# Optimization experiments

Hardware: AMD Instinct MI355X
Metric: run time of the kernel (lower is better)

Reference implementation:

```python
import jax, jax.numpy as jnp
import numpy as np

NUM_USERS = 200000
NUM_ITEMS = 100000
N_NODES = NUM_USERS + NUM_ITEMS
EMB_DIM = 64
N_LAYERS = 3
NNZ = 5000000


def setup_inputs() -> dict:
    key = jax.random.key(0)
    k1, k2, k3, k4, k5 = jax.random.split(key, 5)
    user_emb = 0.1 * jax.random.normal(k1, (NUM_USERS, EMB_DIM), dtype=jnp.float32)
    item_emb = 0.1 * jax.random.normal(k2, (NUM_ITEMS, EMB_DIM), dtype=jnp.float32)
    edge_row = jax.random.randint(k3, (NNZ,), 0, N_NODES, dtype=jnp.int32)
    edge_col = jax.random.randint(k4, (NNZ,), 0, N_NODES, dtype=jnp.int32)
    edge_val = jax.random.uniform(k5, (NNZ,), dtype=jnp.float32)
    return {"user_emb": user_emb, "item_emb": item_emb,
            "edge_row": edge_row, "edge_col": edge_col, "edge_val": edge_val}


def _spmm(edge_row, edge_col, edge_val, x):
    # out[r] = sum_{e: row[e]=r} val[e] * x[col[e]]  (COO SpMM)
    msgs = edge_val[:, None] * x[edge_col]  # [nnz, d]
    return jax.ops.segment_sum(msgs, edge_row, num_segments=N_NODES)


def reference(user_emb, item_emb, edge_row, edge_col, edge_val):
    ego = jnp.concatenate([user_emb, item_emb], axis=0)  # [N, d]
    acc = ego
    h = ego
    for _ in range(N_LAYERS):
        h = _spmm(edge_row, edge_col, edge_val, h)
        acc = acc + h
    mean_emb = acc / jnp.asarray(N_LAYERS + 1, dtype=acc.dtype)
    return mean_emb[:NUM_USERS], mean_emb[NUM_USERS:]
```

## Files before the change

kernel.cpp:

```cpp
#include <hip/hip_runtime.h>
#include <hip/hip_fp16.h>
#include <hip/hip_bf16.h>


#define NUM_USERS 200000
#define NUM_ITEMS 100000
#define N_NODES   300000
#define EMB_DIM   64
#define NNZ       5000000

#define COARSE_SHIFT 10
#define COARSE_ROWS  1024
#define NCOARSE      ((N_NODES + COARSE_ROWS - 1) / COARSE_ROWS)

#define ARENA_CAP 24576

#define P1_CHUNK  16384
#define P1_BLOCKS ((NNZ + P1_CHUNK - 1) / P1_CHUNK)

__global__ void init16_kernel(const float4* __restrict__ user_emb,
                              const float4* __restrict__ item_emb,
                              uint2* __restrict__ h16) {
    const int n4 = N_NODES * (EMB_DIM / 4);
    int idx = blockIdx.x * blockDim.x + threadIdx.x;
    if (idx >= n4) return;
    const int user4 = NUM_USERS * (EMB_DIM / 4);
    float4 v = (idx < user4) ? user_emb[idx] : item_emb[idx - user4];
    __half2 p0 = __floats2half2_rn(v.x, v.y);
    __half2 p1 = __floats2half2_rn(v.z, v.w);
    uint2 u;
    u.x = *(unsigned int*)&p0;
    u.y = *(unsigned int*)&p1;
    h16[idx] = u;
}

__global__ void zero_int_kernel(int* __restrict__ p, int n) {
    int idx = blockIdx.x * blockDim.x + threadIdx.x;
    if (idx < n) p[idx] = 0;
}

__global__ void partition_arena(const int* __restrict__ row,
                                const int* __restrict__ col,
                                const float* __restrict__ val,
                                int* __restrict__ ccur,
                                unsigned long long* __restrict__ arena) {
    __shared__ int hist[NCOARSE];
    __shared__ int lbase[NCOARSE];
    __shared__ int lcur[NCOARSE];
    int t = threadIdx.x;
    int start = blockIdx.x * P1_CHUNK;
    int end = min(start + P1_CHUNK, NNZ);
    for (int j = t; j < NCOARSE; j += 256) { hist[j] = 0; lcur[j] = 0; }
    __syncthreads();
    for (int i = start + t; i < end; i += 256)
        atomicAdd(&hist[(unsigned int)row[i] >> COARSE_SHIFT], 1);
    __syncthreads();
    for (int j = t; j < NCOARSE; j += 256) {
        int c = hist[j];
        if (c > 0)
            lbase[j] = j * ARENA_CAP + atomicAdd(&ccur[j], c);
    }
    __syncthreads();
    for (int i = start + t; i < end; i += 256) {
        int r = row[i];
        int b = (int)((unsigned int)r >> COARSE_SHIFT);
        unsigned int lo = ((unsigned int)col[i] << 10) | ((unsigned int)r & 1023u);
        unsigned long long p = ((unsigned long long)__float_as_uint(val[i]) << 32)
                             | (unsigned long long)lo;
        int pos = lbase[b] + atomicAdd(&lcur[b], 1);
        arena[pos] = p;
    }
}

__global__ void arena_scan(const int* __restrict__ cnt, int* __restrict__ cbase) {
    __shared__ int lds[512];
    int t = threadIdx.x;
    lds[t] = (t < NCOARSE) ? cnt[t] : 0;
    __syncthreads();
    for (int off = 1; off < 512; off <<= 1) {
        int v = (t >= off) ? lds[t - off] : 0;
        __syncthreads();
        lds[t] += v;
        __syncthreads();
    }
    if (t < NCOARSE) cbase[t] = (t > 0) ? lds[t - 1] : 0;
    if (t == 0) cbase[NCOARSE] = lds[NCOARSE - 1];
}

__global__ void __launch_bounds__(1024)
fine_scatter(const int* __restrict__ cbase,
             const int* __restrict__ cnt,
             const unsigned long long* __restrict__ arena,
             unsigned long long* __restrict__ csr,
             int* __restrict__ row_ptr) {
    __shared__ int offs[COARSE_ROWS];
    __shared__ int cur[COARSE_ROWS];
    int t = threadIdx.x;
    int bin = blockIdx.x;
    int n = cnt[bin];
    int cstart = cbase[bin];
    const unsigned long long* src = arena + (size_t)bin * ARENA_CAP;
    offs[t] = 0;
    cur[t] = 0;
    __syncthreads();
    for (int i = t; i < n; i += 1024)
        atomicAdd(&offs[(unsigned int)src[i] & 1023u], 1);
    __syncthreads();
    int c = offs[t];
    for (int off = 1; off < 1024; off <<= 1) {
        int v = (t >= off) ? offs[t - off] : 0;
        __syncthreads();
        offs[t] += v;
        __syncthreads();
    }
    int excl = offs[t] - c;
    __syncthreads();
    offs[t] = excl;
    __syncthreads();
    int r = (bin << COARSE_SHIFT) + t;
    if (r < N_NODES) row_ptr[r] = cstart + excl;
    if (bin == NCOARSE - 1 && t == 0) row_ptr[N_NODES] = cbase[NCOARSE];
    for (int i = t; i < n; i += 1024) {
        unsigned long long p = src[i];
        int rl = (int)((unsigned int)p & 1023u);
        int pos = cstart + offs[rl] + atomicAdd(&cur[rl], 1);
        csr[pos] = p;
    }
}

__global__ void spmm_mid_kernel(const int* __restrict__ row_ptr,
                                const unsigned long long* __restrict__ csr,
                                const __half* __restrict__ x,
                                __half* __restrict__ y) {
    int gid  = blockIdx.x * blockDim.x + threadIdx.x;
    int wid  = gid >> 6;
    int lane = threadIdx.x & 63;
    if (wid >= N_NODES) return;
    wid = __builtin_amdgcn_readfirstlane(wid);
    int s = row_ptr[wid];
    int e = row_ptr[wid + 1];
    float acc = 0.f;
    int k = s;
    for (; k + 8 <= e; k += 8) {
        unsigned long long p0 = csr[k];
        unsigned long long p1 = csr[k + 1];
        unsigned long long p2 = csr[k + 2];
        unsigned long long p3 = csr[k + 3];
        unsigned long long p4 = csr[k + 4];
        unsigned long long p5 = csr[k + 5];
        unsigned long long p6 = csr[k + 6];
        unsigned long long p7 = csr[k + 7];
        float x0 = __half2float(x[(((unsigned int)p0 >> 10) << 6) + lane]);
        float x1 = __half2float(x[(((unsigned int)p1 >> 10) << 6) + lane]);
        float x2 = __half2float(x[(((unsigned int)p2 >> 10) << 6) + lane]);
        float x3 = __half2float(x[(((unsigned int)p3 >> 10) << 6) + lane]);
        float x4 = __half2float(x[(((unsigned int)p4 >> 10) << 6) + lane]);
        float x5 = __half2float(x[(((unsigned int)p5 >> 10) << 6) + lane]);
        float x6 = __half2float(x[(((unsigned int)p6 >> 10) << 6) + lane]);
        float x7 = __half2float(x[(((unsigned int)p7 >> 10) << 6) + lane]);
        acc += __uint_as_float((unsigned int)(p0 >> 32)) * x0;
        acc += __uint_as_float((unsigned int)(p1 >> 32)) * x1;
        acc += __uint_as_float((unsigned int)(p2 >> 32)) * x2;
        acc += __uint_as_float((unsigned int)(p3 >> 32)) * x3;
        acc += __uint_as_float((unsigned int)(p4 >> 32)) * x4;
        acc += __uint_as_float((unsigned int)(p5 >> 32)) * x5;
        acc += __uint_as_float((unsigned int)(p6 >> 32)) * x6;
        acc += __uint_as_float((unsigned int)(p7 >> 32)) * x7;
    }
    for (; k + 4 <= e; k += 4) {
        unsigned long long p0 = csr[k];
        unsigned long long p1 = csr[k + 1];
        unsigned long long p2 = csr[k + 2];
        unsigned long long p3 = csr[k + 3];
        float x0 = __half2float(x[(((unsigned int)p0 >> 10) << 6) + lane]);
        float x1 = __half2float(x[(((unsigned int)p1 >> 10) << 6) + lane]);
        float x2 = __half2float(x[(((unsigned int)p2 >> 10) << 6) + lane]);
        float x3 = __half2float(x[(((unsigned int)p3 >> 10) << 6) + lane]);
        acc += __uint_as_float((unsigned int)(p0 >> 32)) * x0;
        acc += __uint_as_float((unsigned int)(p1 >> 32)) * x1;
        acc += __uint_as_float((unsigned int)(p2 >> 32)) * x2;
        acc += __uint_as_float((unsigned int)(p3 >> 32)) * x3;
    }
    for (; k < e; ++k) {
        unsigned long long p = csr[k];
        acc += __uint_as_float((unsigned int)(p >> 32))
             * __half2float(x[(((unsigned int)p >> 10) << 6) + lane]);
    }
    y[(wid << 6) + lane] = __float2half(acc);
}

__global__ void spmm_last_kernel(const int* __restrict__ row_ptr,
                                 const unsigned long long* __restrict__ csr,
                                 const __half* __restrict__ x,
                                 const __half* __restrict__ h1,
                                 const float* __restrict__ user_emb,
                                 const float* __restrict__ item_emb,
                                 float* __restrict__ out) {
    int gid  = blockIdx.x * blockDim.x + threadIdx.x;
    int wid  = gid >> 6;
    int lane = threadIdx.x & 63;
    if (wid >= N_NODES) return;
    wid = __builtin_amdgcn_readfirstlane(wid);
    int s = row_ptr[wid];
    int e = row_ptr[wid + 1];
    float acc = 0.f;
    int k = s;
    for (; k + 8 <= e; k += 8) {
        unsigned long long p0 = csr[k];
        unsigned long long p1 = csr[k + 1];
        unsigned long long p2 = csr[k + 2];
        unsigned long long p3 = csr[k + 3];
        unsigned long long p4 = csr[k + 4];
        unsigned long long p5 = csr[k + 5];
        unsigned long long p6 = csr[k + 6];
        unsigned long long p7 = csr[k + 7];
        float x0 = __half2float(x[(((unsigned int)p0 >> 10) << 6) + lane]);
        float x1 = __half2float(x[(((unsigned int)p1 >> 10) << 6) + lane]);
        float x2 = __half2float(x[(((unsigned int)p2 >> 10) << 6) + lane]);
        float x3 = __half2float(x[(((unsigned int)p3 >> 10) << 6) + lane]);
        float x4 = __half2float(x[(((unsigned int)p4 >> 10) << 6) + lane]);
        float x5 = __half2float(x[(((unsigned int)p5 >> 10) << 6) + lane]);
        float x6 = __half2float(x[(((unsigned int)p6 >> 10) << 6) + lane]);
        float x7 = __half2float(x[(((unsigned int)p7 >> 10) << 6) + lane]);
        acc += __uint_as_float((unsigned int)(p0 >> 32)) * x0;
        acc += __uint_as_float((unsigned int)(p1 >> 32)) * x1;
        acc += __uint_as_float((unsigned int)(p2 >> 32)) * x2;
        acc += __uint_as_float((unsigned int)(p3 >> 32)) * x3;
        acc += __uint_as_float((unsigned int)(p4 >> 32)) * x4;
        acc += __uint_as_float((unsigned int)(p5 >> 32)) * x5;
        acc += __uint_as_float((unsigned int)(p6 >> 32)) * x6;
        acc += __uint_as_float((unsigned int)(p7 >> 32)) * x7;
    }
    for (; k + 4 <= e; k += 4) {
        unsigned long long p0 = csr[k];
        unsigned long long p1 = csr[k + 1];
        unsigned long long p2 = csr[k + 2];
        unsigned long long p3 = csr[k + 3];
        float x0 = __half2float(x[(((unsigned int)p0 >> 10) << 6) + lane]);
        float x1 = __half2float(x[(((unsigned int)p1 >> 10) << 6) + lane]);
        float x2 = __half2float(x[(((unsigned int)p2 >> 10) << 6) + lane]);
        float x3 = __half2float(x[(((unsigned int)p3 >> 10) << 6) + lane]);
        acc += __uint_as_float((unsigned int)(p0 >> 32)) * x0;
        acc += __uint_as_float((unsigned int)(p1 >> 32)) * x1;
        acc += __uint_as_float((unsigned int)(p2 >> 32)) * x2;
        acc += __uint_as_float((unsigned int)(p3 >> 32)) * x3;
    }
    for (; k < e; ++k) {
        unsigned long long p = csr[k];
        acc += __uint_as_float((unsigned int)(p >> 32))
             * __half2float(x[(((unsigned int)p >> 10) << 6) + lane]);
    }
    int o = (wid << 6) + lane;
    float h0v = (o < NUM_USERS * EMB_DIM) ? user_emb[o]
                                          : item_emb[o - NUM_USERS * EMB_DIM];
    float h1v = __half2float(h1[o]);
    float h2v = __half2float(x[o]);
    __builtin_nontemporal_store((h0v + h1v + h2v + acc) * 0.25f, &out[o]);
}

__global__ void init32_kernel(const float4* __restrict__ user_emb,
                              const float4* __restrict__ item_emb,
                              float4* __restrict__ h,
                              float4* __restrict__ out) {
    const int n4 = N_NODES * (EMB_DIM / 4);
    int idx = blockIdx.x * blockDim.x + threadIdx.x;
    if (idx >= n4) return;
    const int user4 = NUM_USERS * (EMB_DIM / 4);
    float4 v = (idx < user4) ? user_emb[idx] : item_emb[idx - user4];
    h[idx] = v;
    out[idx] = v;
}
__global__ void zero4_kernel(float4* __restrict__ p) {
    const int n4 = N_NODES * (EMB_DIM / 4);
    int idx = blockIdx.x * blockDim.x + threadIdx.x;
    if (idx < n4) p[idx] = make_float4(0.f, 0.f, 0.f, 0.f);
}
__global__ void spmm_push_kernel(const int* __restrict__ row, const int* __restrict__ col,
                                 const float* __restrict__ val, const float* __restrict__ x,
                                 float* __restrict__ y) {
    unsigned int gid = blockIdx.x * blockDim.x + threadIdx.x;
    unsigned int e = gid >> 6, lane = gid & 63u;
    if (e >= NNZ) return;
    atomicAdd(&y[(unsigned int)row[e] * EMB_DIM + lane],
              val[e] * x[(unsigned int)col[e] * EMB_DIM + lane]);
}
__global__ void acc_kernel(float4* __restrict__ out, const float4* __restrict__ h, float scale) {
    const int n4 = N_NODES * (EMB_DIM / 4);
    int idx = blockIdx.x * blockDim.x + threadIdx.x;
    if (idx >= n4) return;
    float4 o = out[idx], a = h[idx];
    o.x = (o.x + a.x) * scale; o.y = (o.y + a.y) * scale;
    o.z = (o.z + a.z) * scale; o.w = (o.w + a.w) * scale;
    out[idx] = o;
}

extern "C" void kernel_launch(void* const* d_in, const int* in_sizes, int n_in,
                              void* d_out, int out_size, void* d_ws, size_t ws_size,
                              hipStream_t stream) {
    const float* user_emb = (const float*)d_in[0];
    const float* item_emb = (const float*)d_in[1];
    const int*   edge_row = (const int*)d_in[2];
    const int*   edge_col = (const int*)d_in[3];
    const float* edge_val = (const float*)d_in[4];
    float* out = (float*)d_out;

    const size_t H16_BYTES = (size_t)N_NODES * EMB_DIM * sizeof(__half);

    char* ws = (char*)d_ws;
    __half* hA     = (__half*)ws;                      ws += H16_BYTES;
    __half* hB     = (__half*)ws;                      ws += H16_BYTES;
    unsigned long long* csr = (unsigned long long*)ws; ws += (size_t)NNZ * 8;
    int*   row_ptr = (int*)ws;                         ws += (size_t)(N_NODES + 4) * 4;
    int*   counts  = (int*)ws;                         ws += (size_t)N_NODES * 4;
    int*   partials= (int*)ws;                         ws += 4096;
    const size_t REQUIRED = (size_t)(ws - (char*)d_ws);

    const int blk     = 256;
    const int n4      = N_NODES * (EMB_DIM / 4);
    const int grid_n4 = (n4 + blk - 1) / blk;

    if (ws_size >= REQUIRED) {
        unsigned long long* arena = (unsigned long long*)hA;
        zero_int_kernel<<<1, 512, 0, stream>>>(counts, NCOARSE);
        partition_arena<<<P1_BLOCKS, 256, 0, stream>>>(
            edge_row, edge_col, edge_val, counts, arena);
        arena_scan<<<1, 512, 0, stream>>>(counts, partials);
        fine_scatter<<<NCOARSE, 1024, 0, stream>>>(partials, counts, arena,
                                                   csr, row_ptr);
        init16_kernel<<<grid_n4, blk, 0, stream>>>(
            (const float4*)user_emb, (const float4*)item_emb, (uint2*)hA);
        const int grid_sp = (int)(((long long)N_NODES * 64) / blk);
        spmm_mid_kernel<<<grid_sp, blk, 0, stream>>>(row_ptr, csr, hA, hB);
        spmm_mid_kernel<<<grid_sp, blk, 0, stream>>>(row_ptr, csr, hB, hA);
        spmm_last_kernel<<<grid_sp, blk, 0, stream>>>(
            row_ptr, csr, hA , hB , user_emb, item_emb, out);
    } else {
        const float scales[3] = {1.0f, 1.0f, 0.25f};
        float* hA32 = (float*)d_ws;
        float* hB32 = hA32 + (size_t)N_NODES * EMB_DIM;
        init32_kernel<<<grid_n4, blk, 0, stream>>>(
            (const float4*)user_emb, (const float4*)item_emb, (float4*)hA32, (float4*)out);
        float* h = hA32; float* hn = hB32;
        const int grid_sp = (int)(((long long)NNZ * 64) / blk);
        for (int layer = 0; layer < 3; ++layer) {
            zero4_kernel<<<grid_n4, blk, 0, stream>>>((float4*)hn);
            spmm_push_kernel<<<grid_sp, blk, 0, stream>>>(edge_row, edge_col, edge_val, h, hn);
            acc_kernel<<<grid_n4, blk, 0, stream>>>((float4*)out, (const float4*)hn, scales[layer]);
            float* t = h; h = hn; hn = t;
        }
    }
}
```

Baseline: 721.2 us.

## Pair rows per wavefront in SpMM and stage fine scatter bins in LDS

Each SpMM wavefront now handles two adjacent rows, interleaving their gather loops to raise memory-level parallelism, and launches half as many waves. The coarse bucket size drops from 1024 to 512 rows, so the column field gets one more bit, the arena capacity is halved, and the scan covers more bins. fine_scatter caches its bin's entries in dynamic shared memory so the arena is read from global memory only once. Interleaving two rows of unequal length adds tail imbalance and register pressure, and bins larger than the cache fall back to the old double-read path.

```diff
diff --git a/kernel.cpp b/kernel.cpp
--- a/kernel.cpp
+++ b/kernel.cpp
@@ -9,14 +9,18 @@
 #define EMB_DIM   64
 #define NNZ       5000000
 
-#define COARSE_SHIFT 10
-#define COARSE_ROWS  1024
+#define COARSE_SHIFT 9
+#define COARSE_ROWS  512
 #define NCOARSE      ((N_NODES + COARSE_ROWS - 1) / COARSE_ROWS)
 
-#define ARENA_CAP 24576
+#define ARENA_CAP 12288
+#define FS_CAP    9216
+#define FS_SHMEM  (FS_CAP * 8 + 2 * COARSE_ROWS * 4)
 
 #define P1_CHUNK  16384
 #define P1_BLOCKS ((NNZ + P1_CHUNK - 1) / P1_CHUNK)
+
+typedef unsigned long long u64;
 
 __global__ void init16_kernel(const float4* __restrict__ user_emb,
                               const float4* __restrict__ item_emb,
@@ -43,7 +47,7 @@
                                 const int* __restrict__ col,
                                 const float* __restrict__ val,
                                 int* __restrict__ ccur,
-                                unsigned long long* __restrict__ arena) {
+                                u64* __restrict__ arena) {
     __shared__ int hist[NCOARSE];
     __shared__ int lbase[NCOARSE];
     __shared__ int lcur[NCOARSE];
@@ -64,20 +68,20 @@
     for (int i = start + t; i < end; i += 256) {
         int r = row[i];
         int b = (int)((unsigned int)r >> COARSE_SHIFT);
-        unsigned int lo = ((unsigned int)col[i] << 10) | ((unsigned int)r & 1023u);
-        unsigned long long p = ((unsigned long long)__float_as_uint(val[i]) << 32)
-                             | (unsigned long long)lo;
+        unsigned int lo = ((unsigned int)col[i] << 9) | ((unsigned int)r & 511u);
+        u64 p = ((u64)__float_as_uint(val[i]) << 32) | (u64)lo;
         int pos = lbase[b] + atomicAdd(&lcur[b], 1);
         arena[pos] = p;
     }
 }
 
-__global__ void arena_scan(const int* __restrict__ cnt, int* __restrict__ cbase) {
-    __shared__ int lds[512];
+__global__ void __launch_bounds__(1024)
+arena_scan(const int* __restrict__ cnt, int* __restrict__ cbase) {
+    __shared__ int lds[1024];
     int t = threadIdx.x;
     lds[t] = (t < NCOARSE) ? cnt[t] : 0;
     __syncthreads();
-    for (int off = 1; off < 512; off <<= 1) {
+    for (int off = 1; off < 1024; off <<= 1) {
         int v = (t >= off) ? lds[t - off] : 0;
         __syncthreads();
         lds[t] += v;
@@ -90,74 +94,88 @@
 __global__ void __launch_bounds__(1024)
 fine_scatter(const int* __restrict__ cbase,
              const int* __restrict__ cnt,
-             const unsigned long long* __restrict__ arena,
-             unsigned long long* __restrict__ csr,
+             const u64* __restrict__ arena,
+             u64* __restrict__ csr,
              int* __restrict__ row_ptr) {
-    __shared__ int offs[COARSE_ROWS];
-    __shared__ int cur[COARSE_ROWS];
+    extern __shared__ u64 smem[];
+    u64* buf  = smem;
+    int* offs = (int*)&smem[FS_CAP];
+    int* cur  = offs + COARSE_ROWS;
     int t = threadIdx.x;
     int bin = blockIdx.x;
     int n = cnt[bin];
     int cstart = cbase[bin];
-    const unsigned long long* src = arena + (size_t)bin * ARENA_CAP;
-    offs[t] = 0;
-    cur[t] = 0;
-    __syncthreads();
-    for (int i = t; i < n; i += 1024)
-        atomicAdd(&offs[(unsigned int)src[i] & 1023u], 1);
-    __syncthreads();
-    int c = offs[t];
-    for (int off = 1; off < 1024; off <<= 1) {
-        int v = (t >= off) ? offs[t - off] : 0;
-        __syncthreads();
-        offs[t] += v;
-        __syncthreads();
-    }
-    int excl = offs[t] - c;
-    __syncthreads();
-    offs[t] = excl;
-    __syncthreads();
-    int r = (bin << COARSE_SHIFT) + t;
-    if (r < N_NODES) row_ptr[r] = cstart + excl;
-    if (bin == NCOARSE - 1 && t == 0) row_ptr[N_NODES] = cbase[NCOARSE];
-    for (int i = t; i < n; i += 1024) {
-        unsigned long long p = src[i];
-        int rl = (int)((unsigned int)p & 1023u);
-        int pos = cstart + offs[rl] + atomicAdd(&cur[rl], 1);
-        csr[pos] = p;
-    }
-}
-
-__global__ void spmm_mid_kernel(const int* __restrict__ row_ptr,
-                                const unsigned long long* __restrict__ csr,
-                                const __half* __restrict__ x,
-                                __half* __restrict__ y) {
-    int gid  = blockIdx.x * blockDim.x + threadIdx.x;
-    int wid  = gid >> 6;
-    int lane = threadIdx.x & 63;
-    if (wid >= N_NODES) return;
-    wid = __builtin_amdgcn_readfirstlane(wid);
-    int s = row_ptr[wid];
-    int e = row_ptr[wid + 1];
-    float acc = 0.f;
-    int k = s;
+    const u64* src = arena + (size_t)bin * ARENA_CAP;
+    if (t < COARSE_ROWS) { offs[t] = 0; cur[t] = 0; }
+    __syncthreads();
+    if (n <= FS_CAP) {
+        for (int i = t; i < n; i += 1024) {
+            u64 p = src[i];
+            buf[i] = p;
+            atomicAdd(&offs[(unsigned int)p & 511u], 1);
+        }
+        __syncthreads();
+        int c = (t < COARSE_ROWS) ? offs[t] : 0;
+        for (int off = 1; off < COARSE_ROWS; off <<= 1) {
+            int v = (t >= off && t < COARSE_ROWS) ? offs[t - off] : 0;
+            __syncthreads();
+            if (t < COARSE_ROWS) offs[t] += v;
+            __syncthreads();
+        }
+        int excl = (t < COARSE_ROWS) ? offs[t] - c : 0;
+        __syncthreads();
+        if (t < COARSE_ROWS) offs[t] = excl;
+        __syncthreads();
+        int r = (bin << COARSE_SHIFT) + t;
+        if (t < COARSE_ROWS && r < N_NODES) row_ptr[r] = cstart + excl;
+        if (bin == NCOARSE - 1 && t == 0) row_ptr[N_NODES] = cbase[NCOARSE];
+        for (int i = t; i < n; i += 1024) {
+            u64 p = buf[i];
+            int rl = (int)((unsigned int)p & 511u);
+            int pos = cstart + offs[rl] + atomicAdd(&cur[rl], 1);
+            csr[pos] = p;
+        }
+    } else {
+        for (int i = t; i < n; i += 1024)
+            atomicAdd(&offs[(unsigned int)src[i] & 511u], 1);
+        __syncthreads();
+        int c = (t < COARSE_ROWS) ? offs[t] : 0;
+        for (int off = 1; off < COARSE_ROWS; off <<= 1) {
+            int v = (t >= off && t < COARSE_ROWS) ? offs[t - off] : 0;
+            __syncthreads();
+            if (t < COARSE_ROWS) offs[t] += v;
+            __syncthreads();
+        }
+        int excl = (t < COARSE_ROWS) ? offs[t] - c : 0;
+        __syncthreads();
+        if (t < COARSE_ROWS) offs[t] = excl;
+        __syncthreads();
+        int r = (bin << COARSE_SHIFT) + t;
+        if (t < COARSE_ROWS && r < N_NODES) row_ptr[r] = cstart + excl;
+        if (bin == NCOARSE - 1 && t == 0) row_ptr[N_NODES] = cbase[NCOARSE];
+        for (int i = t; i < n; i += 1024) {
+            u64 p = src[i];
+            int rl = (int)((unsigned int)p & 511u);
+            int pos = cstart + offs[rl] + atomicAdd(&cur[rl], 1);
+            csr[pos] = p;
+        }
+    }
+}
+
+__device__ __forceinline__ void tail_accum(const u64* __restrict__ csr,
+                                           const __half* __restrict__ x,
+                                           int lane, int k, int e, float& acc) {
     for (; k + 8 <= e; k += 8) {
-        unsigned long long p0 = csr[k];
-        unsigned long long p1 = csr[k + 1];
-        unsigned long long p2 = csr[k + 2];
-        unsigned long long p3 = csr[k + 3];
-        unsigned long long p4 = csr[k + 4];
-        unsigned long long p5 = csr[k + 5];
-        unsigned long long p6 = csr[k + 6];
-        unsigned long long p7 = csr[k + 7];
-        float x0 = __half2float(x[(((unsigned int)p0 >> 10) << 6) + lane]);
-        float x1 = __half2float(x[(((unsigned int)p1 >> 10) << 6) + lane]);
-        float x2 = __half2float(x[(((unsigned int)p2 >> 10) << 6) + lane]);
-        float x3 = __half2float(x[(((unsigned int)p3 >> 10) << 6) + lane]);
-        float x4 = __half2float(x[(((unsigned int)p4 >> 10) << 6) + lane]);
-        float x5 = __half2float(x[(((unsigned int)p5 >> 10) << 6) + lane]);
-        float x6 = __half2float(x[(((unsigned int)p6 >> 10) << 6) + lane]);
-        float x7 = __half2float(x[(((unsigned int)p7 >> 10) << 6) + lane]);
+        u64 p0 = csr[k],     p1 = csr[k + 1], p2 = csr[k + 2], p3 = csr[k + 3];
+        u64 p4 = csr[k + 4], p5 = csr[k + 5], p6 = csr[k + 6], p7 = csr[k + 7];
+        float x0 = __half2float(x[(((unsigned int)p0 >> 9) << 6) + lane]);
+        float x1 = __half2float(x[(((unsigned int)p1 >> 9) << 6) + lane]);
+        float x2 = __half2float(x[(((unsigned int)p2 >> 9) << 6) + lane]);
+        float x3 = __half2float(x[(((unsigned int)p3 >> 9) << 6) + lane]);
+        float x4 = __half2float(x[(((unsigned int)p4 >> 9) << 6) + lane]);
+        float x5 = __half2float(x[(((unsigned int)p5 >> 9) << 6) + lane]);
+        float x6 = __half2float(x[(((unsigned int)p6 >> 9) << 6) + lane]);
+        float x7 = __half2float(x[(((unsigned int)p7 >> 9) << 6) + lane]);
         acc += __uint_as_float((unsigned int)(p0 >> 32)) * x0;
         acc += __uint_as_float((unsigned int)(p1 >> 32)) * x1;
         acc += __uint_as_float((unsigned int)(p2 >> 32)) * x2;
@@ -168,94 +186,115 @@
         acc += __uint_as_float((unsigned int)(p7 >> 32)) * x7;
     }
     for (; k + 4 <= e; k += 4) {
-        unsigned long long p0 = csr[k];
-        unsigned long long p1 = csr[k + 1];
-        unsigned long long p2 = csr[k + 2];
-        unsigned long long p3 = csr[k + 3];
-        float x0 = __half2float(x[(((unsigned int)p0 >> 10) << 6) + lane]);
-        float x1 = __half2float(x[(((unsigned int)p1 >> 10) << 6) + lane]);
-        float x2 = __half2float(x[(((unsigned int)p2 >> 10) << 6) + lane]);
-        float x3 = __half2float(x[(((unsigned int)p3 >> 10) << 6) + lane]);
+        u64 p0 = csr[k], p1 = csr[k + 1], p2 = csr[k + 2], p3 = csr[k + 3];
+        float x0 = __half2float(x[(((unsigned int)p0 >> 9) << 6) + lane]);
+        float x1 = __half2float(x[(((unsigned int)p1 >> 9) << 6) + lane]);
+        float x2 = __half2float(x[(((unsigned int)p2 >> 9) << 6) + lane]);
+        float x3 = __half2float(x[(((unsigned int)p3 >> 9) << 6) + lane]);
         acc += __uint_as_float((unsigned int)(p0 >> 32)) * x0;
         acc += __uint_as_float((unsigned int)(p1 >> 32)) * x1;
         acc += __uint_as_float((unsigned int)(p2 >> 32)) * x2;
         acc += __uint_as_float((unsigned int)(p3 >> 32)) * x3;
     }
     for (; k < e; ++k) {
-        unsigned long long p = csr[k];
+        u64 p = csr[k];
         acc += __uint_as_float((unsigned int)(p >> 32))
-             * __half2float(x[(((unsigned int)p >> 10) << 6) + lane]);
-    }
-    y[(wid << 6) + lane] = __float2half(acc);
+             * __half2float(x[(((unsigned int)p >> 9) << 6) + lane]);
+    }
+}
+
+__device__ __forceinline__ void pair_accum(const int* __restrict__ row_ptr,
+                                           const u64* __restrict__ csr,
+                                           const __half* __restrict__ x,
+                                           int lane, int r0,
+                                           float& acc0, float& acc1) {
+    int s0 = row_ptr[r0];
+    int e0 = row_ptr[r0 + 1];
+    int e1 = row_ptr[r0 + 2];
+    int k0 = s0, k1 = e0;
+    while (k0 + 8 <= e0 && k1 + 8 <= e1) {
+        u64 p0 = csr[k0],     p1 = csr[k0 + 1], p2 = csr[k0 + 2], p3 = csr[k0 + 3];
+        u64 p4 = csr[k0 + 4], p5 = csr[k0 + 5], p6 = csr[k0 + 6], p7 = csr[k0 + 7];
+        u64 q0 = csr[k1],     q1 = csr[k1 + 1], q2 = csr[k1 + 2], q3 = csr[k1 + 3];
+        u64 q4 = csr[k1 + 4], q5 = csr[k1 + 5], q6 = csr[k1 + 6], q7 = csr[k1 + 7];
+        float a0 = __half2float(x[(((unsigned int)p0 >> 9) << 6) + lane]);
+        float a1 = __half2float(x[(((unsigned int)p1 >> 9) << 6) + lane]);
+        float a2 = __half2float(x[(((unsigned int)p2 >> 9) << 6) + lane]);
+        float a3 = __half2float(x[(((unsigned int)p3 >> 9) << 6) + lane]);
+        float a4 = __half2float(x[(((unsigned int)p4 >> 9) << 6) + lane]);
+        float a5 = __half2float(x[(((unsigned int)p5 >> 9) << 6) + lane]);
+        float a6 = __half2float(x[(((unsigned int)p6 >> 9) << 6) + lane]);
+        float a7 = __half2float(x[(((unsigned int)p7 >> 9) << 6) + lane]);
+        float b0 = __half2float(x[(((unsigned int)q0 >> 9) << 6) + lane]);
+        float b1 = __half2float(x[(((unsigned int)q1 >> 9) << 6) + lane]);
+        float b2 = __half2float(x[(((unsigned int)q2 >> 9) << 6) + lane]);
+        float b3 = __half2float(x[(((unsigned int)q3 >> 9) << 6) + lane]);
+        float b4 = __half2float(x[(((unsigned int)q4 >> 9) << 6) + lane]);
+        float b5 = __half2float(x[(((unsigned int)q5 >> 9) << 6) + lane]);
+        float b6 = __half2float(x[(((unsigned int)q6 >> 9) << 6) + lane]);
+        float b7 = __half2float(x[(((unsigned int)q7 >> 9) << 6) + lane]);
+        acc0 += __uint_as_float((unsigned int)(p0 >> 32)) * a0;
+        acc0 += __uint_as_float((unsigned int)(p1 >> 32)) * a1;
+        acc0 += __uint_as_float((unsigned int)(p2 >> 32)) * a2;
+        acc0 += __uint_as_float((unsigned int)(p3 >> 32)) * a3;
+        acc0 += __uint_as_float((unsigned int)(p4 >> 32)) * a4;
+        acc0 += __uint_as_float((unsigned int)(p5 >> 32)) * a5;
+        acc0 += __uint_as_float((unsigned int)(p6 >> 32)) * a6;
+        acc0 += __uint_as_float((unsigned int)(p7 >> 32)) * a7;
+        acc1 += __uint_as_float((unsigned int)(q0 >> 32)) * b0;
+        acc1 += __uint_as_float((unsigned int)(q1 >> 32)) * b1;
+        acc1 += __uint_as_float((unsigned int)(q2 >> 32)) * b2;
+        acc1 += __uint_as_float((unsigned int)(q3 >> 32)) * b3;
+        acc1 += __uint_as_float((unsigned int)(q4 >> 32)) * b4;
+        acc1 += __uint_as_float((unsigned int)(q5 >> 32)) * b5;
+        acc1 += __uint_as_float((unsigned int)(q6 >> 32)) * b6;
+        acc1 += __uint_as_float((unsigned int)(q7 >> 32)) * b7;
+        k0 += 8; k1 += 8;
+    }
+    tail_accum(csr, x, lane, k0, e0, acc0);
+    tail_accum(csr, x, lane, k1, e1, acc1);
+}
+
+__global__ void spmm_mid_kernel(const int* __restrict__ row_ptr,
+                                const u64* __restrict__ csr,
+                                const __half* __restrict__ x,
+                                __half* __restrict__ y) {
+    int gid  = blockIdx.x * blockDim.x + threadIdx.x;
+    int r0   = (gid >> 6) * 2;
+    int lane = threadIdx.x & 63;
+    if (r0 >= N_NODES) return;
+    r0 = __builtin_amdgcn_readfirstlane(r0);
+    float acc0 = 0.f, acc1 = 0.f;
+    pair_accum(row_ptr, csr, x, lane, r0, acc0, acc1);
+    int o = (r0 << 6) + lane;
+    y[o]      = __float2half(acc0);
+    y[o + 64] = __float2half(acc1);
 }
 
 __global__ void spmm_last_kernel(const int* __restrict__ row_ptr,
-                                 const unsigned long long* __restrict__ csr,
+                                 const u64* __restrict__ csr,
                                  const __half* __restrict__ x,
                                  const __half* __restrict__ h1,
                                  const float* __restrict__ user_emb,
                                  const float* __restrict__ item_emb,
                                  float* __restrict__ out) {
     int gid  = blockIdx.x * blockDim.x + threadIdx.x;
-    int wid  = gid >> 6;
+    int r0   = (gid >> 6) * 2;
     int lane = threadIdx.x & 63;
-    if (wid >= N_NODES) return;
-    wid = __builtin_amdgcn_readfirstlane(wid);
-    int s = row_ptr[wid];
-    int e = row_ptr[wid + 1];
-    float acc = 0.f;
-    int k = s;
-    for (; k + 8 <= e; k += 8) {
-        unsigned long long p0 = csr[k];
-        unsigned long long p1 = csr[k + 1];
-        unsigned long long p2 = csr[k + 2];
-        unsigned long long p3 = csr[k + 3];
-        unsigned long long p4 = csr[k + 4];
-        unsigned long long p5 = csr[k + 5];
-        unsigned long long p6 = csr[k + 6];
-        unsigned long long p7 = csr[k + 7];
-        float x0 = __half2float(x[(((unsigned int)p0 >> 10) << 6) + lane]);
-        float x1 = __half2float(x[(((unsigned int)p1 >> 10) << 6) + lane]);
-        float x2 = __half2float(x[(((unsigned int)p2 >> 10) << 6) + lane]);
-        float x3 = __half2float(x[(((unsigned int)p3 >> 10) << 6) + lane]);
-        float x4 = __half2float(x[(((unsigned int)p4 >> 10) << 6) + lane]);
-        float x5 = __half2float(x[(((unsigned int)p5 >> 10) << 6) + lane]);
-        float x6 = __half2float(x[(((unsigned int)p6 >> 10) << 6) + lane]);
-        float x7 = __half2float(x[(((unsigned int)p7 >> 10) << 6) + lane]);
-        acc += __uint_as_float((unsigned int)(p0 >> 32)) * x0;
-        acc += __uint_as_float((unsigned int)(p1 >> 32)) * x1;
-        acc += __uint_as_float((unsigned int)(p2 >> 32)) * x2;
-        acc += __uint_as_float((unsigned int)(p3 >> 32)) * x3;
-        acc += __uint_as_float((unsigned int)(p4 >> 32)) * x4;
-        acc += __uint_as_float((unsigned int)(p5 >> 32)) * x5;
-        acc += __uint_as_float((unsigned int)(p6 >> 32)) * x6;
-        acc += __uint_as_float((unsigned int)(p7 >> 32)) * x7;
-    }
-    for (; k + 4 <= e; k += 4) {
-        unsigned long long p0 = csr[k];
-        unsigned long long p1 = csr[k + 1];
-        unsigned long long p2 = csr[k + 2];
-        unsigned long long p3 = csr[k + 3];
-        float x0 = __half2float(x[(((unsigned int)p0 >> 10) << 6) + lane]);
-        float x1 = __half2float(x[(((unsigned int)p1 >> 10) << 6) + lane]);
-        float x2 = __half2float(x[(((unsigned int)p2 >> 10) << 6) + lane]);
-        float x3 = __half2float(x[(((unsigned int)p3 >> 10) << 6) + lane]);
-        acc += __uint_as_float((unsigned int)(p0 >> 32)) * x0;
-        acc += __uint_as_float((unsigned int)(p1 >> 32)) * x1;
-        acc += __uint_as_float((unsigned int)(p2 >> 32)) * x2;
-        acc += __uint_as_float((unsigned int)(p3 >> 32)) * x3;
-    }
-    for (; k < e; ++k) {
-        unsigned long long p = csr[k];
-        acc += __uint_as_float((unsigned int)(p >> 32))
-             * __half2float(x[(((unsigned int)p >> 10) << 6) + lane]);
-    }
-    int o = (wid << 6) + lane;
-    float h0v = (o < NUM_USERS * EMB_DIM) ? user_emb[o]
-                                          : item_emb[o - NUM_USERS * EMB_DIM];
-    float h1v = __half2float(h1[o]);
-    float h2v = __half2float(x[o]);
-    __builtin_nontemporal_store((h0v + h1v + h2v + acc) * 0.25f, &out[o]);
+    if (r0 >= N_NODES) return;
+    r0 = __builtin_amdgcn_readfirstlane(r0);
+    float acc0 = 0.f, acc1 = 0.f;
+    pair_accum(row_ptr, csr, x, lane, r0, acc0, acc1);
+    int o0 = (r0 << 6) + lane;
+    int o1 = o0 + 64;
+    float h00 = (o0 < NUM_USERS * EMB_DIM) ? user_emb[o0]
+                                           : item_emb[o0 - NUM_USERS * EMB_DIM];
+    float h01 = (o1 < NUM_USERS * EMB_DIM) ? user_emb[o1]
+                                           : item_emb[o1 - NUM_USERS * EMB_DIM];
+    float r0v = (h00 + __half2float(h1[o0]) + __half2float(x[o0]) + acc0) * 0.25f;
+    float r1v = (h01 + __half2float(h1[o1]) + __half2float(x[o1]) + acc1) * 0.25f;
+    __builtin_nontemporal_store(r0v, &out[o0]);
+    __builtin_nontemporal_store(r1v, &out[o1]);
 }
 
 __global__ void init32_kernel(const float4* __restrict__ user_emb,
@@ -309,7 +348,7 @@
     char* ws = (char*)d_ws;
     __half* hA     = (__half*)ws;                      ws += H16_BYTES;
     __half* hB     = (__half*)ws;                      ws += H16_BYTES;
-    unsigned long long* csr = (unsigned long long*)ws; ws += (size_t)NNZ * 8;
+    u64*    csr    = (u64*)ws;                         ws += (size_t)NNZ * 8;
     int*   row_ptr = (int*)ws;                         ws += (size_t)(N_NODES + 4) * 4;
     int*   counts  = (int*)ws;                         ws += (size_t)N_NODES * 4;
     int*   partials= (int*)ws;                         ws += 4096;
@@ -320,16 +359,16 @@
     const int grid_n4 = (n4 + blk - 1) / blk;
 
     if (ws_size >= REQUIRED) {
-        unsigned long long* arena = (unsigned long long*)hA;
-        zero_int_kernel<<<1, 512, 0, stream>>>(counts, NCOARSE);
+        u64* arena = (u64*)hA;
+        zero_int_kernel<<<1, 1024, 0, stream>>>(counts, NCOARSE);
         partition_arena<<<P1_BLOCKS, 256, 0, stream>>>(
             edge_row, edge_col, edge_val, counts, arena);
-        arena_scan<<<1, 512, 0, stream>>>(counts, partials);
-        fine_scatter<<<NCOARSE, 1024, 0, stream>>>(partials, counts, arena,
-                                                   csr, row_ptr);
+        arena_scan<<<1, 1024, 0, stream>>>(counts, partials);
+        fine_scatter<<<NCOARSE, 1024, FS_SHMEM, stream>>>(partials, counts, arena,
+                                                          csr, row_ptr);
         init16_kernel<<<grid_n4, blk, 0, stream>>>(
             (const float4*)user_emb, (const float4*)item_emb, (uint2*)hA);
-        const int grid_sp = (int)(((long long)N_NODES * 64) / blk);
+        const int grid_sp = (int)(((long long)(N_NODES / 2) * 64) / blk);
         spmm_mid_kernel<<<grid_sp, blk, 0, stream>>>(row_ptr, csr, hA, hB);
         spmm_mid_kernel<<<grid_sp, blk, 0, stream>>>(row_ptr, csr, hB, hA);
         spmm_last_kernel<<<grid_sp, blk, 0, stream>>>(
```

Result: faster. 649.9 us (-9.9%).
